# Kernel tuning notes

Hardware: AMD Instinct MI355X
Metric: run time of the kernel (lower is better)

Reference implementation:

```python
import jax, jax.numpy as jnp
import numpy as np


def _prelu(x, a):
    # nn.PReLU() with a single learnable parameter a
    return jnp.where(x >= 0, x, a * x)


def _conv1x1(x, w, b):
    # x: [n, cin, h, w], w: [cout, cin], b: [cout]
    return jnp.einsum('nchw,oc->nohw', x, w) + b[None, :, None, None]


def setup_inputs() -> dict:
    key = jax.random.key(0)
    ks = jax.random.split(key, 7)
    N, C, H, W = 8, 64, 64, 64
    red = 2
    c = C // red
    s = 1.0 / np.sqrt(C).astype(np.float32)
    x = jax.random.normal(ks[0], (N, C, H, W), dtype=jnp.float32)
    w1 = jax.random.normal(ks[1], (c, C), dtype=jnp.float32) * s
    b1 = jnp.zeros((c,), dtype=jnp.float32)
    w2 = jax.random.normal(ks[2], (c, C), dtype=jnp.float32) * s
    b2 = jnp.zeros((c,), dtype=jnp.float32)
    w3 = jax.random.normal(ks[3], (C, C), dtype=jnp.float32) * s
    b3 = jnp.zeros((C,), dtype=jnp.float32)
    a1 = jnp.full((1,), 0.25, dtype=jnp.float32)
    a2 = jnp.full((1,), 0.25, dtype=jnp.float32)
    a3 = jnp.full((1,), 0.25, dtype=jnp.float32)
    return {"x": x, "w1": w1, "b1": b1, "a1": a1, "w2": w2, "b2": b2,
            "a2": a2, "w3": w3, "b3": b3, "a3": a3}


def reference(x, w1, b1, a1, w2, b2, a2, w3, b3, a3):
    res_scale = 1.0
    n, C, h, w = x.shape
    e1 = _prelu(_conv1x1(x, w1, b1), a1[0])  # [n, c, h, w]
    e2 = _prelu(_conv1x1(x, w2, b2), a2[0])  # [n, c, h, w]
    e3 = _prelu(_conv1x1(x, w3, b3), a3[0])  # [n, C, h, w]
    c = e1.shape[1]
    hw = h * w
    q = e1.transpose(0, 2, 3, 1).reshape(n, hw, c)   # [n, hw, c]
    k = e2.reshape(n, c, hw)                         # [n, c, hw]
    score = jax.nn.softmax(jnp.matmul(q, k), axis=-1)  # [n, hw, hw]
    v = e3.reshape(n, C, hw).transpose(0, 2, 1)      # [n, hw, C]
    out = jnp.matmul(score, v)                       # [n, hw, C]
    out = out.transpose(0, 2, 1).reshape(n, C, h, w)
    return out + res_scale * x
```

## Files before the change

kernel.cpp:

```cpp
#include <hip/hip_runtime.h>
#include <hip/hip_bf16.h>

typedef __bf16 bf16x8 __attribute__((ext_vector_type(8)));
typedef float  f32x4  __attribute__((ext_vector_type(4)));
typedef float  f32x16 __attribute__((ext_vector_type(16)));
typedef int    i32x4  __attribute__((ext_vector_type(4)));

#define SEQ 4096
#define CIN 64
#define KBLK 64
#define KSPLIT 8
#define KCHUNK (SEQ / KSPLIT)
#define NTC (KCHUNK / KBLK)
#define LOG2E 1.44269504088896340736f

__device__ __forceinline__ void gll16(const void* g, void* l) {
    __builtin_amdgcn_global_load_lds(
        (const __attribute__((address_space(1))) void*)g,
        (__attribute__((address_space(3))) void*)l, 16, 0, 0);
}

__device__ __forceinline__ unsigned cvtpk(float lo, float hi) {
    unsigned r;
    asm("v_cvt_pk_bf16_f32 %0, %1, %2" : "=v"(r) : "v"(lo), "v"(hi));
    return r;
}

__global__ __launch_bounds__(256, 2) void qkv_gen(
    const float* __restrict__ x,
    const float* __restrict__ w1, const float* __restrict__ b1, const float* __restrict__ a1,
    const float* __restrict__ w2, const float* __restrict__ b2, const float* __restrict__ a2,
    const float* __restrict__ w3, const float* __restrict__ b3, const float* __restrict__ a3,
    __bf16* __restrict__ qws, __bf16* __restrict__ kws, __bf16* __restrict__ vtws)
{
    __shared__ float xs[CIN][64];
    __shared__ float wl[CIN][128];
    __shared__ float bl[128];
    __shared__ float al[4];

    const int t  = threadIdx.x;
    const int n  = blockIdx.x >> 6;
    const int p0 = (blockIdx.x & 63) << 6;

    for (int idx = t; idx < 2048; idx += 256) {
        int j = idx >> 6, c = idx & 63;
        wl[c][j]      = w1[idx];
        wl[c][32 + j] = w2[idx];
    }
    for (int idx = t; idx < 4096; idx += 256) {
        int j = idx >> 6, c = idx & 63;
        wl[c][64 + j] = w3[idx];
    }
    if (t < 32) { bl[t] = b1[t]; bl[32 + t] = b2[t]; }
    if (t >= 128 && t < 192) bl[64 + (t - 128)] = b3[t - 128];
    if (t == 0) { al[0] = a1[0]; al[1] = a2[0]; al[2] = a3[0]; }

    const float* xb = x + ((size_t)n * CIN) * SEQ + p0;
    for (int r = 0; r < 16; ++r) {
        int e = r * 256 + t;
        xs[e >> 6][e & 63] = xb[(size_t)(e >> 6) * SEQ + (e & 63)];
    }
    __syncthreads();

    const int p  = t & 63;
    const int g  = t >> 6;
    const int jb = g << 5;
    const float a = (g == 0) ? al[0] : ((g == 1) ? al[1] : al[2]);

    float acc[32];
    #pragma unroll
    for (int j = 0; j < 32; ++j) acc[j] = bl[jb + j];

    for (int c = 0; c < CIN; ++c) {
        float xv = xs[c][p];
        const f32x4* wr = (const f32x4*)&wl[c][jb];
        #pragma unroll
        for (int j4 = 0; j4 < 8; ++j4) {
            f32x4 wv = wr[j4];
            acc[j4*4+0] = fmaf(wv[0], xv, acc[j4*4+0]);
            acc[j4*4+1] = fmaf(wv[1], xv, acc[j4*4+1]);
            acc[j4*4+2] = fmaf(wv[2], xv, acc[j4*4+2]);
            acc[j4*4+3] = fmaf(wv[3], xv, acc[j4*4+3]);
        }
    }
    #pragma unroll
    for (int j = 0; j < 32; ++j) acc[j] = acc[j] >= 0.f ? acc[j] : a * acc[j];

    const int pg = p0 + p;
    if (g <= 1) {
        const float sc = (g == 0) ? LOG2E : 1.0f;
        __bf16* dst = (g == 0 ? qws : kws) + ((size_t)n * SEQ + pg) * 32;
        #pragma unroll
        for (int v8 = 0; v8 < 4; ++v8) {
            bf16x8 o;
            #pragma unroll
            for (int i = 0; i < 8; ++i) o[i] = (__bf16)(acc[v8*8+i] * sc);
            *(bf16x8*)(dst + v8*8) = o;
        }
    } else {
        __bf16* dst = vtws + ((size_t)n * CIN + (jb - 64)) * SEQ + pg;
        #pragma unroll
        for (int j = 0; j < 32; ++j) dst[(size_t)j * SEQ] = (__bf16)acc[j];
    }
}

template<int ATOMIC>
__global__ __launch_bounds__(256, 4) void attn(
    const __bf16* __restrict__ qws, const __bf16* __restrict__ kws,
    const __bf16* __restrict__ vtws,
    void* __restrict__ Ows, float* __restrict__ lws)
{
    __shared__ __align__(16) char stg[2][12288];

    const int t    = threadIdx.x;
    const int lane = t & 63;
    const int n    = blockIdx.x & 7;
    const int qblk = (blockIdx.x >> 3) & 31;
    const int ks   = blockIdx.x >> 8;
    const int wid  = t >> 6;
    const int l31  = lane & 31;
    const int h    = lane >> 5;
    const int qbase = qblk * 128 + wid * 32;
    const int kbase = ks * KCHUNK;
    const int ksw  = ((l31 >> 1) & 3) << 4;
    const int vsw  = (l31 & 7) << 4;

    const char* kb = (const char*)(kws + (size_t)n * SEQ * 32);
    const char* vb = (const char*)(vtws + (size_t)n * CIN * SEQ);

    const char* qp = (const char*)(qws + (size_t)n * SEQ * 32)
                     + (size_t)(qbase + l31) * 64 + h * 16;
    const bf16x8 qf0 = *(const bf16x8*)(qp);
    const bf16x8 qf1 = *(const bf16x8*)(qp + 32);

    f32x16 of0 = {}, of1 = {};
    float ls = 0.f;

    auto stage = [&](int k0n, int b) {
        {
            int row = t >> 2;
            int c16 = (t & 3) ^ ((t >> 3) & 3);
            gll16(kb + (size_t)(k0n + row) * 64 + c16 * 16, &stg[b][0] + t * 16);
        }
        #pragma unroll
        for (int j = 0; j < 2; ++j) {
            int L   = j * 4096 + t * 16;
            int row = j * 32 + (t >> 3);
            int c16 = (t & 7) ^ ((t >> 3) & 7);
            gll16(vb + (size_t)row * 8192 + (size_t)k0n * 2 + c16 * 16,
                  &stg[b][4096] + L);
        }
    };

    stage(kbase, 0);

    int cur = 0;
    for (int tt = 0; tt < NTC; ++tt) {
        asm volatile("s_waitcnt vmcnt(0)" ::: "memory");
        __builtin_amdgcn_s_barrier();

        if (tt + 1 < NTC) stage(kbase + (tt + 1) * KBLK, cur ^ 1);

        const char* kc_ = &stg[cur][0];
        const char* vc_ = &stg[cur][4096];

        unsigned c0[8], c1[8];

        #pragma unroll
        for (int kti = 0; kti < 2; ++kti) {
            const char* krow = kc_ + (size_t)(kti * 32 + l31) * 64;
            bf16x8 kf0 = *(const bf16x8*)(krow + ((h * 16) ^ ksw));
            bf16x8 kf1 = *(const bf16x8*)(krow + ((32 + h * 16) ^ ksw));
            f32x16 s = {};
            __builtin_amdgcn_s_setprio(1);
            s = __builtin_amdgcn_mfma_f32_32x32x16_bf16(kf0, qf0, s, 0, 0, 0);
            s = __builtin_amdgcn_mfma_f32_32x32x16_bf16(kf1, qf1, s, 0, 0, 0);
            __builtin_amdgcn_s_setprio(0);

            float p[16];
            #pragma unroll
            for (int r = 0; r < 16; ++r) {
                p[r] = __builtin_exp2f(s[r]);
                ls += p[r];
            }
            unsigned* c = kti ? c1 : c0;
            #pragma unroll
            for (int j = 0; j < 4; ++j) {
                c[j]     = cvtpk(p[2*j],     p[2*j + 1]);
                c[4 + j] = cvtpk(p[8 + 2*j], p[9 + 2*j]);
            }
            asm("v_permlane32_swap_b32 %0, %1" : "+v"(c[0]), "+v"(c[2]));
            asm("v_permlane32_swap_b32 %0, %1" : "+v"(c[1]), "+v"(c[3]));
            asm("v_permlane32_swap_b32 %0, %1" : "+v"(c[4]), "+v"(c[6]));
            asm("v_permlane32_swap_b32 %0, %1" : "+v"(c[5]), "+v"(c[7]));
        }

        __builtin_amdgcn_s_setprio(1);
        #pragma unroll
        for (int s4 = 0; s4 < 4; ++s4) {
            const unsigned* cs = (s4 < 2) ? c0 : c1;
            const int sl = (s4 & 1) * 4;
            i32x4 bi = { (int)cs[sl], (int)cs[sl+1], (int)cs[sl+2], (int)cs[sl+3] };
            bf16x8 pf = __builtin_bit_cast(bf16x8, bi);
            const int colv = (s4 * 32 + h * 16) ^ vsw;
            bf16x8 vf0 = *(const bf16x8*)(vc_ + (size_t)l31 * 128 + colv);
            bf16x8 vf1 = *(const bf16x8*)(vc_ + (size_t)(32 + l31) * 128 + colv);
            of0 = __builtin_amdgcn_mfma_f32_32x32x16_bf16(vf0, pf, of0, 0, 0, 0);
            of1 = __builtin_amdgcn_mfma_f32_32x32x16_bf16(vf1, pf, of1, 0, 0, 0);
        }
        __builtin_amdgcn_s_setprio(0);

        cur ^= 1;
    }

    const int qg = qbase + l31;
    if (ATOMIC) {
        float* Ob = (float*)Ows + (size_t)n * CIN * SEQ;
        #pragma unroll
        for (int r = 0; r < 16; ++r) {
            int dv = (r & 3) + 8 * (r >> 2) + 4 * h;
            unsafeAtomicAdd(Ob + (size_t)dv * SEQ + qg,        of0[r]);
            unsafeAtomicAdd(Ob + (size_t)(dv + 32) * SEQ + qg, of1[r]);
        }
        unsafeAtomicAdd(lws + n * SEQ + qg, ls);
    } else {
        __bf16* Ob = (__bf16*)Ows + (size_t)ks * (8 * CIN * SEQ) + (size_t)n * CIN * SEQ;
        #pragma unroll
        for (int r = 0; r < 16; ++r) {
            int dv = (r & 3) + 8 * (r >> 2) + 4 * h;
            Ob[(size_t)dv * SEQ + qg]        = (__bf16)of0[r];
            Ob[(size_t)(dv + 32) * SEQ + qg] = (__bf16)of1[r];
        }
        float lt = ls + __shfl_xor(ls, 32);
        if (h == 0) lws[(size_t)ks * (8 * SEQ) + n * SEQ + qg] = lt;
    }
}

__global__ __launch_bounds__(256) void lred(float* __restrict__ lws)
{
    int i = blockIdx.x * 256 + threadIdx.x;
    float s = 0.f;
    #pragma unroll
    for (int ks = 0; ks < KSPLIT; ++ks) s += lws[ks * 32768 + i];
    lws[i] = 1.f / s;
}

__global__ __launch_bounds__(256) void combine8(
    const __bf16* __restrict__ O8, const float* __restrict__ linv,
    const float* __restrict__ x, float* __restrict__ out)
{
    const int i = blockIdx.x * 256 + threadIdx.x;
    const int q8 = i & 511;
    const int nd = i >> 9;
    const int n  = nd >> 6;

    float o[8] = {};
    const __bf16* base = O8 + (size_t)nd * SEQ + q8 * 8;
    #pragma unroll
    for (int ks = 0; ks < KSPLIT; ++ks) {
        bf16x8 v = *(const bf16x8*)(base + (size_t)ks * (8 * CIN * SEQ));
        #pragma unroll
        for (int j = 0; j < 8; ++j) o[j] += (float)v[j];
    }
    const float* ivp = linv + n * SEQ + q8 * 8;
    f32x4 iv0 = *(const f32x4*)(ivp);
    f32x4 iv1 = *(const f32x4*)(ivp + 4);
    const float* xp = x + (size_t)nd * SEQ + q8 * 8;
    f32x4 x0 = *(const f32x4*)(xp);
    f32x4 x1 = *(const f32x4*)(xp + 4);
    f32x4 r0, r1;
    r0[0] = o[0]*iv0[0] + x0[0]; r0[1] = o[1]*iv0[1] + x0[1];
    r0[2] = o[2]*iv0[2] + x0[2]; r0[3] = o[3]*iv0[3] + x0[3];
    r1[0] = o[4]*iv1[0] + x1[0]; r1[1] = o[5]*iv1[1] + x1[1];
    r1[2] = o[6]*iv1[2] + x1[2]; r1[3] = o[7]*iv1[3] + x1[3];
    float* op = out + (size_t)nd * SEQ + q8 * 8;
    *(f32x4*)(op)     = r0;
    *(f32x4*)(op + 4) = r1;
}

__global__ __launch_bounds__(256) void combine1(
    const float* __restrict__ Ows, const float* __restrict__ lws,
    const float* __restrict__ x, float* __restrict__ out)
{
    const int total = 8 * CIN * SEQ / 4;
    for (int i = blockIdx.x * 256 + threadIdx.x; i < total; i += gridDim.x * 256) {
        int q4 = i & 1023;
        int n  = i >> 16;
        f32x4 o4 = *(const f32x4*)(Ows + (size_t)i * 4);
        f32x4 l4 = *(const f32x4*)(lws + (size_t)n * SEQ + q4 * 4);
        f32x4 x4 = *(const f32x4*)(x + (size_t)i * 4);
        f32x4 r;
        r[0] = o4[0] / l4[0] + x4[0];
        r[1] = o4[1] / l4[1] + x4[1];
        r[2] = o4[2] / l4[2] + x4[2];
        r[3] = o4[3] / l4[3] + x4[3];
        *(f32x4*)(out + (size_t)i * 4) = r;
    }
}

extern "C" void kernel_launch(void* const* d_in, const int* in_sizes, int n_in,
                              void* d_out, int out_size, void* d_ws, size_t ws_size,
                              hipStream_t stream)
{
    (void)in_sizes; (void)n_in; (void)out_size;
    const float* x  = (const float*)d_in[0];
    const float* w1 = (const float*)d_in[1];
    const float* b1 = (const float*)d_in[2];
    const float* a1 = (const float*)d_in[3];
    const float* w2 = (const float*)d_in[4];
    const float* b2 = (const float*)d_in[5];
    const float* a2 = (const float*)d_in[6];
    const float* w3 = (const float*)d_in[7];
    const float* b3 = (const float*)d_in[8];
    const float* a3 = (const float*)d_in[9];
    float* out = (float*)d_out;

    char* ws = (char*)d_ws;
    __bf16* qws  = (__bf16*)(ws);
    __bf16* kws  = (__bf16*)(ws + (2u << 20));
    __bf16* vtws = (__bf16*)(ws + (4u << 20));

    hipLaunchKernelGGL(qkv_gen, dim3(512), dim3(256), 0, stream,
                       x, w1, b1, a1, w2, b2, a2, w3, b3, a3, qws, kws, vtws);

    const size_t need_split = (8u << 20) + (32u << 20) + (1u << 20);
    if (ws_size >= need_split) {
        __bf16* O8   = (__bf16*)(ws + (8u << 20));
        float*  lws8 = (float*)(ws + (40u << 20));
        hipLaunchKernelGGL(attn<0>, dim3(8 * 32 * KSPLIT), dim3(256), 0, stream,
                           qws, kws, vtws, (void*)O8, lws8);
        hipLaunchKernelGGL(lred, dim3(128), dim3(256), 0, stream, lws8);
        hipLaunchKernelGGL(combine8, dim3(1024), dim3(256), 0, stream,
                           O8, lws8, x, out);
    } else {
        float* Ows = (float*)(ws + (8u << 20));
        float* lws = (float*)(ws + (16u << 20));
        hipMemsetAsync(Ows, 0, (8u << 20) + (128u << 10), stream);
        hipLaunchKernelGGL(attn<1>, dim3(8 * 32 * KSPLIT), dim3(256), 0, stream,
                           qws, kws, vtws, (void*)Ows, lws);
        hipLaunchKernelGGL(combine1, dim3(1024), dim3(256), 0, stream,
                           Ows, lws, x, out);
    }
}
```

Measured before the change: 82.80 us.

## Load K/V fragments directly from global memory with MFMA-ready V layout

The V workspace is rewritten in a tiled layout of 16 positions by 64 channels, so each lane's bf16x8 fragment is a contiguous 16-byte global load. The attention kernel drops the LDS double-buffered staging, the barriers and the swizzles, and reads K and V fragments straight from global (L2-cached) memory each iteration. This removes LDS traffic and block-wide synchronization, but loses the explicit prefetch overlap and the cross-wave sharing of loaded tiles, and it also removes the s_setprio hints.

```diff
diff --git a/kernel.cpp b/kernel.cpp
--- a/kernel.cpp
+++ b/kernel.cpp
@@ -14,12 +14,6 @@
 #define NTC (KCHUNK / KBLK)
 #define LOG2E 1.44269504088896340736f
 
-__device__ __forceinline__ void gll16(const void* g, void* l) {
-    __builtin_amdgcn_global_load_lds(
-        (const __attribute__((address_space(1))) void*)g,
-        (__attribute__((address_space(3))) void*)l, 16, 0, 0);
-}
-
 __device__ __forceinline__ unsigned cvtpk(float lo, float hi) {
     unsigned r;
     asm("v_cvt_pk_bf16_f32 %0, %1, %2" : "=v"(r) : "v"(lo), "v"(hi));
@@ -98,9 +92,10 @@
             *(bf16x8*)(dst + v8*8) = o;
         }
     } else {
-        __bf16* dst = vtws + ((size_t)n * CIN + (jb - 64)) * SEQ + pg;
-        #pragma unroll
-        for (int j = 0; j < 32; ++j) dst[(size_t)j * SEQ] = (__bf16)acc[j];
+        __bf16* dst = vtws + (size_t)n * (256 * 1024)
+                      + (size_t)(pg >> 4) * 1024 + (jb - 64) * 16 + (pg & 15);
+        #pragma unroll
+        for (int j = 0; j < 32; ++j) dst[j * 16] = (__bf16)acc[j];
     }
 }
 
@@ -110,8 +105,6 @@
     const __bf16* __restrict__ vtws,
     void* __restrict__ Ows, float* __restrict__ lws)
 {
-    __shared__ __align__(16) char stg[2][12288];
-
     const int t    = threadIdx.x;
     const int lane = t & 63;
     const int n    = blockIdx.x & 7;
@@ -122,11 +115,9 @@
     const int h    = lane >> 5;
     const int qbase = qblk * 128 + wid * 32;
     const int kbase = ks * KCHUNK;
-    const int ksw  = ((l31 >> 1) & 3) << 4;
-    const int vsw  = (l31 & 7) << 4;
 
     const char* kb = (const char*)(kws + (size_t)n * SEQ * 32);
-    const char* vb = (const char*)(vtws + (size_t)n * CIN * SEQ);
+    const char* vb = (const char*)(vtws + (size_t)n * (256 * 1024));
 
     const char* qp = (const char*)(qws + (size_t)n * SEQ * 32)
                      + (size_t)(qbase + l31) * 64 + h * 16;
@@ -136,81 +127,65 @@
     f32x16 of0 = {}, of1 = {};
     float ls = 0.f;
 
-    auto stage = [&](int k0n, int b) {
+    for (int tt = 0; tt < NTC; ++tt) {
+        const int k0 = kbase + tt * KBLK;
+        const char* kp = kb + (size_t)k0 * 64;
+        const char* vp = vb + (size_t)(k0 >> 4) * 2048;
+
+        bf16x8 kf0a = *(const bf16x8*)(kp + l31 * 64 + h * 16);
+        bf16x8 kf1a = *(const bf16x8*)(kp + l31 * 64 + 32 + h * 16);
+        bf16x8 kf0b = *(const bf16x8*)(kp + (32 + l31) * 64 + h * 16);
+        bf16x8 kf1b = *(const bf16x8*)(kp + (32 + l31) * 64 + 32 + h * 16);
+
+        unsigned c0[8], c1[8];
+
         {
-            int row = t >> 2;
-            int c16 = (t & 3) ^ ((t >> 3) & 3);
-            gll16(kb + (size_t)(k0n + row) * 64 + c16 * 16, &stg[b][0] + t * 16);
-        }
-        #pragma unroll
-        for (int j = 0; j < 2; ++j) {
-            int L   = j * 4096 + t * 16;
-            int row = j * 32 + (t >> 3);
-            int c16 = (t & 7) ^ ((t >> 3) & 7);
-            gll16(vb + (size_t)row * 8192 + (size_t)k0n * 2 + c16 * 16,
-                  &stg[b][4096] + L);
-        }
-    };
-
-    stage(kbase, 0);
-
-    int cur = 0;
-    for (int tt = 0; tt < NTC; ++tt) {
-        asm volatile("s_waitcnt vmcnt(0)" ::: "memory");
-        __builtin_amdgcn_s_barrier();
-
-        if (tt + 1 < NTC) stage(kbase + (tt + 1) * KBLK, cur ^ 1);
-
-        const char* kc_ = &stg[cur][0];
-        const char* vc_ = &stg[cur][4096];
-
-        unsigned c0[8], c1[8];
-
-        #pragma unroll
-        for (int kti = 0; kti < 2; ++kti) {
-            const char* krow = kc_ + (size_t)(kti * 32 + l31) * 64;
-            bf16x8 kf0 = *(const bf16x8*)(krow + ((h * 16) ^ ksw));
-            bf16x8 kf1 = *(const bf16x8*)(krow + ((32 + h * 16) ^ ksw));
             f32x16 s = {};
-            __builtin_amdgcn_s_setprio(1);
-            s = __builtin_amdgcn_mfma_f32_32x32x16_bf16(kf0, qf0, s, 0, 0, 0);
-            s = __builtin_amdgcn_mfma_f32_32x32x16_bf16(kf1, qf1, s, 0, 0, 0);
-            __builtin_amdgcn_s_setprio(0);
-
+            s = __builtin_amdgcn_mfma_f32_32x32x16_bf16(kf0a, qf0, s, 0, 0, 0);
+            s = __builtin_amdgcn_mfma_f32_32x32x16_bf16(kf1a, qf1, s, 0, 0, 0);
             float p[16];
             #pragma unroll
-            for (int r = 0; r < 16; ++r) {
-                p[r] = __builtin_exp2f(s[r]);
-                ls += p[r];
+            for (int r = 0; r < 16; ++r) { p[r] = __builtin_exp2f(s[r]); ls += p[r]; }
+            #pragma unroll
+            for (int j = 0; j < 4; ++j) {
+                c0[j]     = cvtpk(p[2*j],     p[2*j + 1]);
+                c0[4 + j] = cvtpk(p[8 + 2*j], p[9 + 2*j]);
             }
-            unsigned* c = kti ? c1 : c0;
+            asm("v_permlane32_swap_b32 %0, %1" : "+v"(c0[0]), "+v"(c0[2]));
+            asm("v_permlane32_swap_b32 %0, %1" : "+v"(c0[1]), "+v"(c0[3]));
+            asm("v_permlane32_swap_b32 %0, %1" : "+v"(c0[4]), "+v"(c0[6]));
+            asm("v_permlane32_swap_b32 %0, %1" : "+v"(c0[5]), "+v"(c0[7]));
+        }
+        {
+            f32x16 s = {};
+            s = __builtin_amdgcn_mfma_f32_32x32x16_bf16(kf0b, qf0, s, 0, 0, 0);
+            s = __builtin_amdgcn_mfma_f32_32x32x16_bf16(kf1b, qf1, s, 0, 0, 0);
+            float p[16];
+            #pragma unroll
+            for (int r = 0; r < 16; ++r) { p[r] = __builtin_exp2f(s[r]); ls += p[r]; }
             #pragma unroll
             for (int j = 0; j < 4; ++j) {
-                c[j]     = cvtpk(p[2*j],     p[2*j + 1]);
-                c[4 + j] = cvtpk(p[8 + 2*j], p[9 + 2*j]);
+                c1[j]     = cvtpk(p[2*j],     p[2*j + 1]);
+                c1[4 + j] = cvtpk(p[8 + 2*j], p[9 + 2*j]);
             }
-            asm("v_permlane32_swap_b32 %0, %1" : "+v"(c[0]), "+v"(c[2]));
-            asm("v_permlane32_swap_b32 %0, %1" : "+v"(c[1]), "+v"(c[3]));
-            asm("v_permlane32_swap_b32 %0, %1" : "+v"(c[4]), "+v"(c[6]));
-            asm("v_permlane32_swap_b32 %0, %1" : "+v"(c[5]), "+v"(c[7]));
-        }
-
-        __builtin_amdgcn_s_setprio(1);
+            asm("v_permlane32_swap_b32 %0, %1" : "+v"(c1[0]), "+v"(c1[2]));
+            asm("v_permlane32_swap_b32 %0, %1" : "+v"(c1[1]), "+v"(c1[3]));
+            asm("v_permlane32_swap_b32 %0, %1" : "+v"(c1[4]), "+v"(c1[6]));
+            asm("v_permlane32_swap_b32 %0, %1" : "+v"(c1[5]), "+v"(c1[7]));
+        }
+
         #pragma unroll
         for (int s4 = 0; s4 < 4; ++s4) {
             const unsigned* cs = (s4 < 2) ? c0 : c1;
             const int sl = (s4 & 1) * 4;
             i32x4 bi = { (int)cs[sl], (int)cs[sl+1], (int)cs[sl+2], (int)cs[sl+3] };
             bf16x8 pf = __builtin_bit_cast(bf16x8, bi);
-            const int colv = (s4 * 32 + h * 16) ^ vsw;
-            bf16x8 vf0 = *(const bf16x8*)(vc_ + (size_t)l31 * 128 + colv);
-            bf16x8 vf1 = *(const bf16x8*)(vc_ + (size_t)(32 + l31) * 128 + colv);
+            const char* vt_ = vp + s4 * 2048 + l31 * 32 + h * 16;
+            bf16x8 vf0 = *(const bf16x8*)(vt_);
+            bf16x8 vf1 = *(const bf16x8*)(vt_ + 1024);
             of0 = __builtin_amdgcn_mfma_f32_32x32x16_bf16(vf0, pf, of0, 0, 0, 0);
             of1 = __builtin_amdgcn_mfma_f32_32x32x16_bf16(vf1, pf, of1, 0, 0, 0);
         }
-        __builtin_amdgcn_s_setprio(0);
-
-        cur ^= 1;
     }
 
     const int qg = qbase + l31;
```

Result: slower. 85.79 us (+3.6%).
